# Kernel optimization log

Hardware: AMD Instinct MI355X
Metric: run time of the kernel (lower is better)

The kernel has to match this reference:

```python
import jax, jax.numpy as jnp
import numpy as np

V = 16384      # total nodes
G = 32         # nodes per graph (512 graphs)
D = 256        # node embedding dim == hidden_size
N = 8          # heads
H = 32         # head size
I = 1024       # intermediate size
LN_EPS = 1e-12


def _layer_norm(x, g, b):
    mu = jnp.mean(x, axis=-1, keepdims=True)
    var = jnp.mean(jnp.square(x - mu), axis=-1, keepdims=True)
    return (x - mu) * jax.lax.rsqrt(var + LN_EPS) * g + b


def setup_inputs() -> dict:
    key = jax.random.key(0)
    ks = jax.random.split(key, 5)
    node_embeddings = jax.random.normal(ks[0], (V, D), jnp.float32)
    # fully-connected pairs within each graph of size G (sorted by source node)
    idx = np.arange(V, dtype=np.int32).reshape(-1, G)          # [num_graphs, G]
    src = np.repeat(idx, G, axis=1).reshape(-1)                # [P]
    dst = np.tile(idx, (1, G)).reshape(-1)                     # [P]
    in_graph_node_pairs = jnp.asarray(np.stack([src, dst], axis=-1))  # [P, 2]
    s = 0.02
    return {
        "node_embeddings": node_embeddings,
        "in_graph_node_pairs": in_graph_node_pairs,
        "W_qkv": jax.random.normal(ks[1], (D, 3 * N * H), jnp.float32) * s,
        "W_o": jax.random.normal(ks[2], (N * H, D), jnp.float32) * s,
        "ln1_g": jnp.ones((D,), jnp.float32),
        "ln1_b": jnp.zeros((D,), jnp.float32),
        "W_i": jax.random.normal(ks[3], (D, I), jnp.float32) * s,
        "W_out2": jax.random.normal(ks[4], (I, D), jnp.float32) * s,
        "ln2_g": jnp.ones((D,), jnp.float32),
        "ln2_b": jnp.zeros((D,), jnp.float32),
    }


def reference(node_embeddings, in_graph_node_pairs, W_qkv, W_o, ln1_g, ln1_b,
              W_i, W_out2, ln2_g, ln2_b):
    nV = node_embeddings.shape[0]
    src = in_graph_node_pairs[:, 0]
    dst = in_graph_node_pairs[:, 1]
    # QKV projection -> [V, N, 3H] -> split
    qkv = (node_embeddings @ W_qkv).reshape(nV, N, 3 * H)
    q, k, v = jnp.split(qkv, 3, axis=-1)                       # each [V, N, H]
    # per-pair scores [P, N]
    scores = jnp.einsum('phi,phi->ph', q[src], k[dst]) / jnp.sqrt(jnp.float32(H))
    # segment softmax over source node, all heads at once
    m = jax.ops.segment_max(scores, src, num_segments=nV)       # [V, N]
    e = jnp.exp(scores - m[src])
    denom = jax.ops.segment_sum(e, src, num_segments=nV)        # [V, N]
    w = e / denom[src]                                          # [P, N]
    # weighted value scatter-sum -> [V, N, H]
    wv = w[:, :, None] * v[dst]
    att = jax.ops.segment_sum(wv, src, num_segments=nV).reshape(nV, N * H)
    # output projection + residual + LN
    pre = _layer_norm(att @ W_o + node_embeddings, ln1_g, ln1_b)
    inter = jax.nn.gelu(pre @ W_i, approximate=False)
    out = _layer_norm(inter @ W_out2 + pre, ln2_g, ln2_b)
    return out
```

## Files before the change

### kernel.cpp

```cpp
#include <hip/hip_runtime.h>
#include <math.h>

#define V 16384
#define D 256
#define NH 256
#define THREE_NH 768
#define IDIM 1024
#define LN_EPS 1e-12f
#define SCL 0.17677669529663687f

typedef short s16x8 __attribute__((ext_vector_type(8)));
typedef float f32x4 __attribute__((ext_vector_type(4)));

__device__ inline unsigned short f2bf(float f) {
    unsigned u = __float_as_uint(f);
    u += 0x7fffu + ((u >> 16) & 1u);
    return (unsigned short)(u >> 16);
}
__device__ inline float bf2f(unsigned short s) {
    return __uint_as_float(((unsigned)s) << 16);
}

__device__ inline float fast_erf(float x) {
    float ax = fabsf(x);
    float t  = 1.f / fmaf(0.3275911f, ax, 1.f);
    float p  = fmaf(fmaf(fmaf(fmaf(1.061405429f, t, -1.453152027f), t,
                              1.421413741f), t, -0.284496736f), t, 0.254829592f);
    float e  = 1.f - p * t * __expf(-ax * ax);
    return copysignf(e, x);
}

__device__ inline void gl2lds16(const unsigned short* g, unsigned short* l) {
    __builtin_amdgcn_global_load_lds(
        (__attribute__((address_space(1))) void*)(g),
        (__attribute__((address_space(3))) void*)(l), 16, 0, 0);
}

template <int ROWS_T>
__device__ inline void stage(const unsigned short* __restrict__ src, size_t row0,
                             int ldk, int k0, unsigned short* lds, int wv, int lane) {
    constexpr int PER_WAVE = ROWS_T / 32;
    #pragma unroll
    for (int i = 0; i < PER_WAVE; ++i) {
        const int seg = wv * PER_WAVE + i;
        const int r = seg * 8 + (lane >> 3);
        const int c = (lane & 7) ^ (r & 7);
        gl2lds16(src + (row0 + (size_t)r) * ldk + k0 + c * 8, lds + seg * 512);
    }
}

__device__ inline s16x8 fragld(const unsigned short* lds, int row, int chunk) {
    return *(const s16x8*)&lds[row * 64 + ((chunk ^ (row & 7)) << 3)];
}

__global__ __launch_bounds__(256) void prep(const float* __restrict__ X,
                                            unsigned short* __restrict__ Xb,
                                            const float* __restrict__ Wqkv,
                                            const float* __restrict__ Wo,
                                            const float* __restrict__ Wi,
                                            const float* __restrict__ Wo2,
                                            unsigned short* __restrict__ WqkvT,
                                            unsigned short* __restrict__ WoT,
                                            unsigned short* __restrict__ WiT,
                                            unsigned short* __restrict__ Wo2T) {
    const int b = blockIdx.x, t = threadIdx.x;
    if (b >= 768) {
        int i = (b - 768) * 256 + t;
        float4 v = ((const float4*)X)[i];
        ushort4 o;
        o.x = f2bf(v.x); o.y = f2bf(v.y); o.z = f2bf(v.z); o.w = f2bf(v.w);
        ((ushort4*)Xb)[i] = o;
        return;
    }
    __shared__ float tile[32][33];
    const float* W; unsigned short* Wt; int K, N, bx, by;
    if (b < 192)      { W = Wqkv; Wt = WqkvT; K = 256;  N = 768;  bx = b & 7;          by = b >> 3; }
    else if (b < 256) { W = Wo;   Wt = WoT;   K = 256;  N = 256;  bx = (b - 192) & 7;  by = (b - 192) >> 3; }
    else if (b < 512) { W = Wi;   Wt = WiT;   K = 256;  N = 1024; bx = (b - 256) & 7;  by = (b - 256) >> 3; }
    else              { W = Wo2;  Wt = Wo2T;  K = 1024; N = 256;  bx = (b - 512) & 31; by = (b - 512) >> 5; }
    const int k0 = bx * 32, n0 = by * 32;
    #pragma unroll
    for (int p = 0; p < 4; ++p) {
        int idx = t + p * 256, r = idx >> 5, c = idx & 31;
        tile[r][c] = W[(size_t)(k0 + r) * N + n0 + c];
    }
    __syncthreads();
    #pragma unroll
    for (int p = 0; p < 4; ++p) {
        int idx = t + p * 256, r = idx >> 5, c = idx & 31;
        Wt[(size_t)(n0 + r) * K + k0 + c] = f2bf(tile[c][r]);
    }
}

template <int K, int N, int EPI>
__global__ __launch_bounds__(256) void gemm128(const unsigned short* __restrict__ A,
                                               const unsigned short* __restrict__ Bt,
                                               unsigned short* __restrict__ C) {
    __shared__ unsigned short As[128 * 64];
    __shared__ unsigned short Bs[128 * 64];
    constexpr int NCOL = N / 128;
    const int b = blockIdx.x;
    const int idx = b >> 3;
    const int r0 = ((b & 7) * 16 + idx / NCOL) * 128;
    const int c0 = (idx % NCOL) * 128;
    const int t = threadIdx.x;
    const int wv = t >> 6, lane = t & 63, q = lane >> 4, l16 = lane & 15;
    const int wr = (wv >> 1) * 64, wc = (wv & 1) * 64;
    f32x4 acc[4][4] = {};

    for (int k0 = 0; k0 < K; k0 += 64) {
        __syncthreads();
        stage<128>(A,  (size_t)r0, K, k0, As, wv, lane);
        stage<128>(Bt, (size_t)c0, K, k0, Bs, wv, lane);
        __builtin_amdgcn_s_waitcnt(0);
        __syncthreads();
        #pragma unroll
        for (int kk2 = 0; kk2 < 2; ++kk2) {
            s16x8 af[4], bfr[4];
            #pragma unroll
            for (int mf = 0; mf < 4; ++mf)
                af[mf] = fragld(As, wr + mf * 16 + l16, kk2 * 4 + q);
            #pragma unroll
            for (int nf = 0; nf < 4; ++nf)
                bfr[nf] = fragld(Bs, wc + nf * 16 + l16, kk2 * 4 + q);
            #pragma unroll
            for (int mf = 0; mf < 4; ++mf)
                #pragma unroll
                for (int nf = 0; nf < 4; ++nf)
                    acc[mf][nf] = __builtin_amdgcn_mfma_f32_16x16x32_bf16(af[mf], bfr[nf], acc[mf][nf], 0, 0, 0);
        }
    }

    #pragma unroll
    for (int mf = 0; mf < 4; ++mf)
        #pragma unroll
        for (int nf = 0; nf < 4; ++nf) {
            const int cg = c0 + wc + nf * 16 + l16;
            #pragma unroll
            for (int r = 0; r < 4; ++r) {
                const int rg = r0 + wr + mf * 16 + q * 4 + r;
                float v = acc[mf][nf][r];
                if (EPI == 1) v = 0.5f * v * (1.f + fast_erf(v * 0.70710678118654752f));
                C[(size_t)rg * N + cg] = f2bf(v);
            }
        }
}

__global__ __launch_bounds__(256) void ffn_ln(const unsigned short* __restrict__ preb,
                                              const unsigned short* __restrict__ WiT,
                                              const unsigned short* __restrict__ Wo2T,
                                              const float* __restrict__ gamma,
                                              const float* __restrict__ beta,
                                              float* __restrict__ out) {
    __shared__ unsigned short Apre[32 * 64 * 4];
    __shared__ unsigned short Pbuf[32 * 64 * 4];
    __shared__ float2 partial[4][32];
    __shared__ float2 stats[32];
    const int t = threadIdx.x, r0 = blockIdx.x * 32;
    const int wv = t >> 6, lane = t & 63, q = lane >> 4, l16 = lane & 15;
    const int wc = wv * 64;
    f32x4 acc2[2][4] = {};

    #pragma unroll
    for (int kc = 0; kc < 4; ++kc)
        stage<32>(preb, (size_t)r0, 256, kc * 64, Apre + kc * 2048, wv, lane);
    __builtin_amdgcn_s_waitcnt(0);
    __syncthreads();

    const unsigned short* Bp2 = Wo2T + (size_t)(wc + l16) * IDIM;

    for (int nc = 0; nc < 4; ++nc) {
        const unsigned short* Bp1 = WiT + (size_t)(nc * 256 + wc + l16) * 256;
        f32x4 acc1[2][4] = {};
        #pragma unroll
        for (int k0 = 0; k0 < 256; k0 += 64) {
            const unsigned short* Ak = Apre + (k0 >> 6) * 2048;
            #pragma unroll
            for (int kk2 = 0; kk2 < 2; ++kk2) {
                s16x8 af[2], bv[4];
                #pragma unroll
                for (int mf = 0; mf < 2; ++mf)
                    af[mf] = fragld(Ak, mf * 16 + l16, kk2 * 4 + q);
                #pragma unroll
                for (int nf = 0; nf < 4; ++nf)
                    bv[nf] = *(const s16x8*)&Bp1[(size_t)nf * 16 * 256 + k0 + (kk2 * 4 + q) * 8];
                #pragma unroll
                for (int mf = 0; mf < 2; ++mf)
                    #pragma unroll
                    for (int nf = 0; nf < 4; ++nf)
                        acc1[mf][nf] = __builtin_amdgcn_mfma_f32_16x16x32_bf16(af[mf], bv[nf], acc1[mf][nf], 0, 0, 0);
            }
        }

        #pragma unroll
        for (int mf = 0; mf < 2; ++mf)
            #pragma unroll
            for (int nf = 0; nf < 4; ++nf)
                #pragma unroll
                for (int r = 0; r < 4; ++r) {
                    float v = acc1[mf][nf][r];
                    v = 0.5f * v * (1.f + fast_erf(v * 0.70710678118654752f));
                    const int i = mf * 16 + q * 4 + r;
                    const int colc = wc + nf * 16 + l16;
                    const int c8 = (colc >> 3) & 7;
                    Pbuf[wv * 2048 + i * 64 + ((c8 ^ (i & 7)) << 3) + (colc & 7)] = f2bf(v);
                }
        __syncthreads();

        #pragma unroll
        for (int ks = 0; ks < 256; ks += 64) {
            const unsigned short* Pk = Pbuf + (ks >> 6) * 2048;
            #pragma unroll
            for (int kk2 = 0; kk2 < 2; ++kk2) {
                s16x8 af[2], bv[4];
                #pragma unroll
                for (int mf = 0; mf < 2; ++mf)
                    af[mf] = fragld(Pk, mf * 16 + l16, kk2 * 4 + q);
                #pragma unroll
                for (int nf = 0; nf < 4; ++nf)
                    bv[nf] = *(const s16x8*)&Bp2[(size_t)nf * 16 * IDIM + nc * 256 + ks + (kk2 * 4 + q) * 8];
                #pragma unroll
                for (int mf = 0; mf < 2; ++mf)
                    #pragma unroll
                    for (int nf = 0; nf < 4; ++nf)
                        acc2[mf][nf] = __builtin_amdgcn_mfma_f32_16x16x32_bf16(af[mf], bv[nf], acc2[mf][nf], 0, 0, 0);
            }
        }
        __syncthreads();
    }

    #pragma unroll
    for (int mf = 0; mf < 2; ++mf)
        #pragma unroll
        for (int nf = 0; nf < 4; ++nf) {
            const int cg = wc + nf * 16 + l16;
            const int kb = cg >> 6, c8 = (cg >> 3) & 7, e = cg & 7;
            #pragma unroll
            for (int r = 0; r < 4; ++r) {
                const int i = mf * 16 + q * 4 + r;
                acc2[mf][nf][r] += bf2f(Apre[kb * 2048 + i * 64 + ((c8 ^ (i & 7)) << 3) + e]);
            }
        }

    #pragma unroll
    for (int mf = 0; mf < 2; ++mf) {
        float s[4] = {0.f, 0.f, 0.f, 0.f}, ss[4] = {0.f, 0.f, 0.f, 0.f};
        #pragma unroll
        for (int nf = 0; nf < 4; ++nf)
            #pragma unroll
            for (int r = 0; r < 4; ++r) {
                float v = acc2[mf][nf][r];
                s[r] += v; ss[r] += v * v;
            }
        #pragma unroll
        for (int off = 1; off < 16; off <<= 1)
            #pragma unroll
            for (int r = 0; r < 4; ++r) {
                s[r]  += __shfl_xor(s[r],  off);
                ss[r] += __shfl_xor(ss[r], off);
            }
        if (l16 == 0)
            #pragma unroll
            for (int r = 0; r < 4; ++r)
                partial[wv][mf * 16 + q * 4 + r] = make_float2(s[r], ss[r]);
    }
    __syncthreads();
    if (t < 32) {
        float s = 0.f, ss = 0.f;
        #pragma unroll
        for (int w = 0; w < 4; ++w) { s += partial[w][t].x; ss += partial[w][t].y; }
        float mu  = s * (1.f / 256.f);
        float var = ss * (1.f / 256.f) - mu * mu;
        stats[t] = make_float2(mu, rsqrtf(var + LN_EPS));
    }
    __syncthreads();

    #pragma unroll
    for (int mf = 0; mf < 2; ++mf)
        #pragma unroll
        for (int nf = 0; nf < 4; ++nf) {
            const int cg = wc + nf * 16 + l16;
            const float g = gamma[cg], b = beta[cg];
            #pragma unroll
            for (int r = 0; r < 4; ++r) {
                const int rl = mf * 16 + q * 4 + r;
                const float2 st = stats[rl];
                out[(size_t)(r0 + rl) * NH + cg] = (acc2[mf][nf][r] - st.x) * st.y * g + b;
            }
        }
}

__global__ __launch_bounds__(256) void attln(const unsigned short* __restrict__ qkv,
                                             const unsigned short* __restrict__ WoT,
                                             const float* __restrict__ X,
                                             const float* __restrict__ gamma,
                                             const float* __restrict__ beta,
                                             unsigned short* __restrict__ preb) {
    __shared__ unsigned short smem[25216];
    unsigned short* Ks = smem;
    unsigned short* Vt = smem + 8192;
    unsigned short* Ps = smem + 16384;
    unsigned short* at = smem;
    float2* partial = (float2*)(smem + 24576);
    float2* stats   = (float2*)(smem + 24576 + 512);

    const int g = blockIdx.x, t = threadIdx.x;
    const int wv = t >> 6, lane = t & 63, q = lane >> 4, l16 = lane & 15;
    const unsigned short* src = qkv + (size_t)g * 32 * THREE_NH;

    s16x8 qf[2][2];
    #pragma unroll
    for (int hh = 0; hh < 2; ++hh)
        #pragma unroll
        for (int mf = 0; mf < 2; ++mf)
            qf[hh][mf] = *(const s16x8*)&src[(size_t)(mf * 16 + l16) * THREE_NH +
                                             (wv * 2 + hh) * 96 + q * 8];

    s16x8 vld[4];
    int vh[4], vj[4], vdc[4];
    #pragma unroll
    for (int i = 0; i < 4; ++i) {
        int cid = i * 256 + t;
        vh[i] = cid >> 7; int rem = cid & 127; vj[i] = rem >> 2; vdc[i] = rem & 3;
        vld[i] = *(const s16x8*)&src[(size_t)vj[i] * THREE_NH + vh[i] * 96 + 64 + vdc[i] * 8];
    }

    #pragma unroll
    for (int i = 0; i < 4; ++i) {
        int ck = (wv * 4 + i) * 64 + lane;
        int h = ck >> 7, j = (ck >> 2) & 31, c = ck & 3;
        gl2lds16(src + (size_t)j * THREE_NH + h * 96 + 32 + c * 8, Ks + (wv * 4 + i) * 512);
    }

    #pragma unroll
    for (int i = 0; i < 4; ++i)
        #pragma unroll
        for (int e = 0; e < 8; ++e) {
            int d = vdc[i] * 8 + e;
            Vt[vh[i] * 1024 + d * 32 + ((((vj[i] >> 3) ^ ((d >> 2) & 3))) << 3) + (vj[i] & 7)] =
                (unsigned short)vld[i][e];
        }

    __builtin_amdgcn_s_waitcnt(0);
    __syncthreads();

    f32x4 sacc[2][2][2] = {};
    #pragma unroll
    for (int hh = 0; hh < 2; ++hh) {
        const int h = wv * 2 + hh;
        #pragma unroll
        for (int nf = 0; nf < 2; ++nf) {
            s16x8 kf = *(const s16x8*)&Ks[h * 1024 + (nf * 16 + l16) * 32 + q * 8];
            #pragma unroll
            for (int mf = 0; mf < 2; ++mf)
                sacc[hh][mf][nf] = __builtin_amdgcn_mfma_f32_16x16x32_bf16(
                    qf[hh][mf], kf, sacc[hh][mf][nf], 0, 0, 0);
        }
    }

    float inv[2][2][4];
    #pragma unroll
    for (int hh = 0; hh < 2; ++hh) {
        const int h = wv * 2 + hh;
        #pragma unroll
        for (int mf = 0; mf < 2; ++mf)
            #pragma unroll
            for (int r = 0; r < 4; ++r) {
                float a0 = sacc[hh][mf][0][r], a1 = sacc[hh][mf][1][r];
                float m = fmaxf(a0, a1);
                m = fmaxf(m, __shfl_xor(m, 1));
                m = fmaxf(m, __shfl_xor(m, 2));
                m = fmaxf(m, __shfl_xor(m, 4));
                m = fmaxf(m, __shfl_xor(m, 8));
                float e0 = __expf((a0 - m) * SCL);
                float e1 = __expf((a1 - m) * SCL);
                float sm = e0 + e1;
                sm += __shfl_xor(sm, 1);
                sm += __shfl_xor(sm, 2);
                sm += __shfl_xor(sm, 4);
                sm += __shfl_xor(sm, 8);
                inv[hh][mf][r] = 1.f / sm;
                const int row = mf * 16 + q * 4 + r;
                const int base = h * 1024 + row * 32 + (l16 & 7);
                Ps[base + ((((l16 >> 3) ^ q)) << 3)]       = f2bf(e0);
                Ps[base + ((((2 + (l16 >> 3)) ^ q)) << 3)] = f2bf(e1);
            }
    }

    f32x4 oacc[2][2][2] = {};
    #pragma unroll
    for (int hh = 0; hh < 2; ++hh) {
        const int h = wv * 2 + hh;
        const int sw = (l16 >> 2) & 3;
        s16x8 pa[2], vb[2];
        #pragma unroll
        for (int mf = 0; mf < 2; ++mf)
            pa[mf] = *(const s16x8*)&Ps[h * 1024 + (mf * 16 + l16) * 32 + ((q ^ sw) << 3)];
        #pragma unroll
        for (int nf = 0; nf < 2; ++nf)
            vb[nf] = *(const s16x8*)&Vt[h * 1024 + (nf * 16 + l16) * 32 + ((q ^ sw) << 3)];
        #pragma unroll
        for (int mf = 0; mf < 2; ++mf)
            #pragma unroll
            for (int nf = 0; nf < 2; ++nf)
                oacc[hh][mf][nf] = __builtin_amdgcn_mfma_f32_16x16x32_bf16(
                    pa[mf], vb[nf], oacc[hh][mf][nf], 0, 0, 0);
    }
    __syncthreads();

    #pragma unroll
    for (int hh = 0; hh < 2; ++hh)
        #pragma unroll
        for (int mf = 0; mf < 2; ++mf)
            #pragma unroll
            for (int nf = 0; nf < 2; ++nf)
                #pragma unroll
                for (int r = 0; r < 4; ++r) {
                    float val = oacc[hh][mf][nf][r] * inv[hh][mf][r];
                    const int i = mf * 16 + q * 4 + r;
                    const int col = (wv * 2 + hh) * 32 + nf * 16 + l16;
                    const int kb = col >> 6, c = (col >> 3) & 7;
                    at[kb * 2048 + i * 64 + ((c ^ (i & 7)) << 3) + (col & 7)] = f2bf(val);
                }
    __syncthreads();

    const int wc = wv * 64;
    const int r0 = g * 32;
    f32x4 acc[2][4] = {};
    const unsigned short* Bp = WoT + (size_t)(wc + l16) * NH;

    #pragma unroll
    for (int kc = 0; kc < 4; ++kc) {
        const unsigned short* atk = at + kc * 2048;
        #pragma unroll
        for (int kk2 = 0; kk2 < 2; ++kk2) {
            s16x8 af[2], bv[4];
            #pragma unroll
            for (int mf = 0; mf < 2; ++mf)
                af[mf] = fragld(atk, mf * 16 + l16, kk2 * 4 + q);
            #pragma unroll
            for (int nf = 0; nf < 4; ++nf)
                bv[nf] = *(const s16x8*)&Bp[(size_t)nf * 16 * NH + kc * 64 + (kk2 * 4 + q) * 8];
            #pragma unroll
            for (int mf = 0; mf < 2; ++mf)
                #pragma unroll
                for (int nf = 0; nf < 4; ++nf)
                    acc[mf][nf] = __builtin_amdgcn_mfma_f32_16x16x32_bf16(af[mf], bv[nf], acc[mf][nf], 0, 0, 0);
        }
    }

    #pragma unroll
    for (int mf = 0; mf < 2; ++mf)
        #pragma unroll
        for (int nf = 0; nf < 4; ++nf) {
            const int cg = wc + nf * 16 + l16;
            #pragma unroll
            for (int r = 0; r < 4; ++r)
                acc[mf][nf][r] += X[(size_t)(r0 + mf * 16 + q * 4 + r) * NH + cg];
        }

    #pragma unroll
    for (int mf = 0; mf < 2; ++mf) {
        float sp[4] = {0.f, 0.f, 0.f, 0.f}, ssp[4] = {0.f, 0.f, 0.f, 0.f};
        #pragma unroll
        for (int nf = 0; nf < 4; ++nf)
            #pragma unroll
            for (int r = 0; r < 4; ++r) {
                float v = acc[mf][nf][r];
                sp[r] += v; ssp[r] += v * v;
            }
        #pragma unroll
        for (int off = 1; off < 16; off <<= 1)
            #pragma unroll
            for (int r = 0; r < 4; ++r) {
                sp[r]  += __shfl_xor(sp[r],  off);
                ssp[r] += __shfl_xor(ssp[r], off);
            }
        if (l16 == 0)
            #pragma unroll
            for (int r = 0; r < 4; ++r)
                partial[wv * 32 + mf * 16 + q * 4 + r] = make_float2(sp[r], ssp[r]);
    }
    __syncthreads();
    if (t < 32) {
        float sv = 0.f, ssv = 0.f;
        #pragma unroll
        for (int w = 0; w < 4; ++w) { sv += partial[w * 32 + t].x; ssv += partial[w * 32 + t].y; }
        float mu  = sv * (1.f / 256.f);
        float var = ssv * (1.f / 256.f) - mu * mu;
        stats[t] = make_float2(mu, rsqrtf(var + LN_EPS));
    }
    __syncthreads();

    #pragma unroll
    for (int mf = 0; mf < 2; ++mf)
        #pragma unroll
        for (int nf = 0; nf < 4; ++nf) {
            const int cg = wc + nf * 16 + l16;
            const float gm = gamma[cg], bt = beta[cg];
            #pragma unroll
            for (int r = 0; r < 4; ++r) {
                const int rl = mf * 16 + q * 4 + r;
                const float2 st = stats[rl];
                float v = (acc[mf][nf][r] - st.x) * st.y * gm + bt;
                preb[(size_t)(r0 + rl) * NH + cg] = f2bf(v);
            }
        }
}

extern "C" void kernel_launch(void* const* d_in, const int* in_sizes, int n_in,
                              void* d_out, int out_size, void* d_ws, size_t ws_size,
                              hipStream_t stream) {
    const float* X      = (const float*)d_in[0];
    const float* W_qkv  = (const float*)d_in[2];
    const float* W_o    = (const float*)d_in[3];
    const float* ln1_g  = (const float*)d_in[4];
    const float* ln1_b  = (const float*)d_in[5];
    const float* W_i    = (const float*)d_in[6];
    const float* W_out2 = (const float*)d_in[7];
    const float* ln2_g  = (const float*)d_in[8];
    const float* ln2_b  = (const float*)d_in[9];
    float* out = (float*)d_out;

    char* ws = (char*)d_ws;
    unsigned short* Xbf   = (unsigned short*)(ws);
    unsigned short* qkvb  = (unsigned short*)(ws + 8388608);
    unsigned short* preb  = (unsigned short*)(ws + 58720256);
    unsigned short* WqkvT = (unsigned short*)(ws + 67108864);
    unsigned short* WoT   = (unsigned short*)(ws + 67502080);
    unsigned short* WiT   = (unsigned short*)(ws + 67633152);
    unsigned short* Wo2T  = (unsigned short*)(ws + 68157440);

    dim3 blk(256);
    hipLaunchKernelGGL(prep, dim3(768 + V * D / 4 / 256), blk, 0, stream,
                       X, Xbf, W_qkv, W_o, W_i, W_out2, WqkvT, WoT, WiT, Wo2T);

    hipLaunchKernelGGL((gemm128<D, THREE_NH, 0>), dim3(V / 128 * (THREE_NH / 128)), blk, 0, stream,
                       Xbf, WqkvT, qkvb);
    hipLaunchKernelGGL(attln, dim3(V / 32), blk, 0, stream,
                       qkvb, WoT, X, ln1_g, ln1_b, preb);
    hipLaunchKernelGGL(ffn_ln, dim3(V / 32), blk, 0, stream,
                       preb, WiT, Wo2T, ln2_g, ln2_b, out);
}
```

Before: 185.6 us.

## Stage weight B-tiles into per-wave LDS via global_load_lds in FFN and attention-out GEMMs

The B operands of the fused FFN kernel (WiT, Wo2T) and the attention output projection (WoT) were read as 16-byte fragments straight from global memory inside the MFMA loops. They are now copied per wave into a private swizzled LDS segment with async global-to-LDS loads and read back with the conflict-free fragld pattern. Per-wave waitcnt fences replace block barriers. The copies are not double-buffered, so each k-step serialises load then compute, and the FFN kernel's LDS footprint grows, which can lower occupancy.

```diff
diff --git a/kernel.cpp b/kernel.cpp
--- a/kernel.cpp
+++ b/kernel.cpp
@@ -49,9 +49,24 @@
     }
 }
 
+__device__ inline void stage_wp(const unsigned short* __restrict__ src, size_t row0,
+                                int ldk, int k0, unsigned short* seg, int lane) {
+    #pragma unroll
+    for (int i = 0; i < 8; ++i) {
+        const int r = i * 8 + (lane >> 3);
+        const int c = (lane & 7) ^ (r & 7);
+        gl2lds16(src + (row0 + (size_t)r) * ldk + k0 + c * 8, seg + i * 512);
+    }
+}
+
 __device__ inline s16x8 fragld(const unsigned short* lds, int row, int chunk) {
     return *(const s16x8*)&lds[row * 64 + ((chunk ^ (row & 7)) << 3)];
 }
+
+#define WAVE_LGKM0() do { asm volatile("s_waitcnt lgkmcnt(0)" ::: "memory"); \
+                          __builtin_amdgcn_sched_barrier(0); } while (0)
+#define WAVE_VM0()   do { asm volatile("s_waitcnt vmcnt(0)" ::: "memory");   \
+                          __builtin_amdgcn_sched_barrier(0); } while (0)
 
 __global__ __launch_bounds__(256) void prep(const float* __restrict__ X,
                                             unsigned short* __restrict__ Xb,
@@ -152,13 +167,15 @@
                                               const float* __restrict__ gamma,
                                               const float* __restrict__ beta,
                                               float* __restrict__ out) {
-    __shared__ unsigned short Apre[32 * 64 * 4];
-    __shared__ unsigned short Pbuf[32 * 64 * 4];
+    __shared__ unsigned short Apre[8192];
+    __shared__ unsigned short Bs[16384];
+    __shared__ unsigned short Pbuf[8192];
     __shared__ float2 partial[4][32];
     __shared__ float2 stats[32];
     const int t = threadIdx.x, r0 = blockIdx.x * 32;
     const int wv = t >> 6, lane = t & 63, q = lane >> 4, l16 = lane & 15;
     const int wc = wv * 64;
+    unsigned short* Bseg = Bs + wv * 4096;
     f32x4 acc2[2][4] = {};
 
     #pragma unroll
@@ -167,13 +184,13 @@
     __builtin_amdgcn_s_waitcnt(0);
     __syncthreads();
 
-    const unsigned short* Bp2 = Wo2T + (size_t)(wc + l16) * IDIM;
-
     for (int nc = 0; nc < 4; ++nc) {
-        const unsigned short* Bp1 = WiT + (size_t)(nc * 256 + wc + l16) * 256;
         f32x4 acc1[2][4] = {};
         #pragma unroll
         for (int k0 = 0; k0 < 256; k0 += 64) {
+            WAVE_LGKM0();
+            stage_wp(WiT, (size_t)(nc * 256 + wc), 256, k0, Bseg, lane);
+            WAVE_VM0();
             const unsigned short* Ak = Apre + (k0 >> 6) * 2048;
             #pragma unroll
             for (int kk2 = 0; kk2 < 2; ++kk2) {
@@ -183,7 +200,7 @@
                     af[mf] = fragld(Ak, mf * 16 + l16, kk2 * 4 + q);
                 #pragma unroll
                 for (int nf = 0; nf < 4; ++nf)
-                    bv[nf] = *(const s16x8*)&Bp1[(size_t)nf * 16 * 256 + k0 + (kk2 * 4 + q) * 8];
+                    bv[nf] = fragld(Bseg, nf * 16 + l16, kk2 * 4 + q);
                 #pragma unroll
                 for (int mf = 0; mf < 2; ++mf)
                     #pragma unroll
@@ -209,6 +226,9 @@
 
         #pragma unroll
         for (int ks = 0; ks < 256; ks += 64) {
+            WAVE_LGKM0();
+            stage_wp(Wo2T, (size_t)wc, IDIM, nc * 256 + ks, Bseg, lane);
+            WAVE_VM0();
             const unsigned short* Pk = Pbuf + (ks >> 6) * 2048;
             #pragma unroll
             for (int kk2 = 0; kk2 < 2; ++kk2) {
@@ -218,7 +238,7 @@
                     af[mf] = fragld(Pk, mf * 16 + l16, kk2 * 4 + q);
                 #pragma unroll
                 for (int nf = 0; nf < 4; ++nf)
-                    bv[nf] = *(const s16x8*)&Bp2[(size_t)nf * 16 * IDIM + nc * 256 + ks + (kk2 * 4 + q) * 8];
+                    bv[nf] = fragld(Bseg, nf * 16 + l16, kk2 * 4 + q);
                 #pragma unroll
                 for (int mf = 0; mf < 2; ++mf)
                     #pragma unroll
@@ -301,6 +321,7 @@
     unsigned short* Vt = smem + 8192;
     unsigned short* Ps = smem + 16384;
     unsigned short* at = smem;
+    unsigned short* Bs = smem + 8192;
     float2* partial = (float2*)(smem + 24576);
     float2* stats   = (float2*)(smem + 24576 + 512);
 
@@ -426,11 +447,14 @@
 
     const int wc = wv * 64;
     const int r0 = g * 32;
+    unsigned short* Bseg = Bs + wv * 4096;
     f32x4 acc[2][4] = {};
-    const unsigned short* Bp = WoT + (size_t)(wc + l16) * NH;
 
     #pragma unroll
     for (int kc = 0; kc < 4; ++kc) {
+        WAVE_LGKM0();
+        stage_wp(WoT, (size_t)wc, 256, kc * 64, Bseg, lane);
+        WAVE_VM0();
         const unsigned short* atk = at + kc * 2048;
         #pragma unroll
         for (int kk2 = 0; kk2 < 2; ++kk2) {
@@ -440,7 +464,7 @@
                 af[mf] = fragld(atk, mf * 16 + l16, kk2 * 4 + q);
             #pragma unroll
             for (int nf = 0; nf < 4; ++nf)
-                bv[nf] = *(const s16x8*)&Bp[(size_t)nf * 16 * NH + kc * 64 + (kk2 * 4 + q) * 8];
+                bv[nf] = fragld(Bseg, nf * 16 + l16, kk2 * 4 + q);
             #pragma unroll
             for (int mf = 0; mf < 2; ++mf)
                 #pragma unroll
```

Measured after the change: 153.7 us. 1.21x faster.
